# Kernel optimization log

Measured on AMD Instinct MI355X. Metric: run time of the kernel, lower is better.

Reference implementation:

```python
import jax, jax.numpy as jnp
import numpy as np

B, S, D, H = 4, 2048, 1024, 16
DEPTH = D // H
NEG = 1e10


def setup_inputs() -> dict:
    key = jax.random.key(0)
    ks = jax.random.split(key, 11)
    sc = 0.02
    return {
        "q": jax.random.normal(ks[0], (B, S, D), jnp.float32),
        "v": jax.random.normal(ks[1], (B, S, D), jnp.float32),
        "k": jax.random.normal(ks[2], (B, S, D), jnp.float32),
        "Wq": jax.random.normal(ks[3], (D, D), jnp.float32) * sc,
        "bq": jnp.zeros((D,), jnp.float32),
        "Wk": jax.random.normal(ks[4], (D, D), jnp.float32) * sc,
        "bk": jnp.zeros((D,), jnp.float32),
        "Wv": jax.random.normal(ks[5], (D, D), jnp.float32) * sc,
        "bv": jnp.zeros((D,), jnp.float32),
        "Wo": jax.random.normal(ks[6], (D, D), jnp.float32) * sc,
        "bo": jnp.zeros((D,), jnp.float32),
        "mask": 1,
    }


def _split_heads(x):
    # [B, S, D] -> [B, H, S, depth]
    b, s, _ = x.shape
    return x.reshape(b, s, H, DEPTH).transpose(0, 2, 1, 3)


def reference(q, v, k, Wq, bq, Wk, bk, Wv, bv, Wo, bo, mask):
    qh = _split_heads(q @ Wq + bq)
    kh = _split_heads(k @ Wk + bk)
    vh = _split_heads(v @ Wv + bv)

    scale = 1.0 / jnp.sqrt(jnp.asarray(DEPTH, jnp.float32))
    # [B, H, Sq, Sk]
    logits = jnp.einsum("bhqd,bhkd->bhqk", qh, kh) * scale

    if mask:
        nd, ns = logits.shape[-2], logits.shape[-1]
        i = jnp.arange(nd)[:, None]
        j = jnp.arange(ns)[None, :]
        b = (i >= j - ns + nd).astype(logits.dtype)  # lower triangle from lower-right
        logits = logits * b - NEG * (1.0 - b)

    attn = jax.nn.softmax(logits, axis=-1)
    out = jnp.einsum("bhqk,bhkd->bhqd", attn, vh)  # [B, H, Sq, depth]
    out = out.transpose(0, 2, 1, 3).reshape(q.shape[0], -1, D)  # concat heads
    return out @ Wo + bo
```

## Files before the change

### kernel.cpp

```cpp
#include <hip/hip_runtime.h>
#include <hip/hip_bf16.h>
#include <cstdint>
#include <cstddef>

#define S_LEN 2048
#define D_MODEL 1024
#define N_HEADS 16
#define DEPTH 64
#define BATCH 4

#define GLOBAL_AS __attribute__((address_space(1)))
#define LDS_AS __attribute__((address_space(3)))

typedef __attribute__((ext_vector_type(4))) float f32x4;
typedef __attribute__((ext_vector_type(8))) short bf16x8;
typedef __attribute__((ext_vector_type(4))) unsigned short us4;
typedef __attribute__((ext_vector_type(8))) unsigned short us8;

__device__ __forceinline__ unsigned short f2bf(float f) {
  unsigned int u = __builtin_bit_cast(unsigned int, f);
  u += 0x7FFFu + ((u >> 16) & 1u);
  return (unsigned short)(u >> 16);
}

__device__ __forceinline__ unsigned short f2bf_hw(float f) {
  return __builtin_bit_cast(unsigned short, __float2bfloat16(f));
}

__global__ __launch_bounds__(256) void transpose_cast(const float* __restrict__ W,
                                                      unsigned short* __restrict__ Wt,
                                                      int N, float scale) {
  __shared__ float tile[32][33];
  int bx = blockIdx.x * 32;
  int by = blockIdx.y * 32;
  int tx = threadIdx.x, ty = threadIdx.y;
#pragma unroll
  for (int i = 0; i < 4; ++i)
    tile[ty + i * 8][tx] = W[(size_t)(by + ty + i * 8) * N + bx + tx];
  __syncthreads();
#pragma unroll
  for (int i = 0; i < 4; ++i)
    Wt[(size_t)(bx + ty + i * 8) * N + by + tx] = f2bf(tile[tx][ty + i * 8] * scale);
}

__global__ __launch_bounds__(256) void transpose_v(const unsigned short* __restrict__ Vp,
                                                   unsigned short* __restrict__ Vt) {
  __shared__ unsigned short tile[64][72];
  int tid = threadIdx.x;
  int sb = blockIdx.x;
  int bh = blockIdx.y;
  int b = bh >> 4, h = bh & 15;
  int s0 = sb * 64;
#pragma unroll
  for (int rep = 0; rep < 2; ++rep) {
    int idx = rep * 256 + tid;
    int r = idx >> 3, c8 = idx & 7;
    us8 v = *(const us8*)(Vp + (size_t)(b * S_LEN + s0 + r) * D_MODEL + h * DEPTH + c8 * 8);
#pragma unroll
    for (int e = 0; e < 8; ++e) tile[c8 * 8 + e][r] = v[e];
  }
  __syncthreads();
#pragma unroll
  for (int rep = 0; rep < 2; ++rep) {
    int idx = rep * 256 + tid;
    int d = idx >> 3, c8 = idx & 7;
    us8 v = *(const us8*)&tile[d][c8 * 8];
    *(us8*)(Vt + ((size_t)(bh * DEPTH + d)) * S_LEN + s0 + c8 * 8) = v;
  }
}

struct GemmSlice {
  const void* A;
  const unsigned short* Bt;
  const float* bias;
  void* C;
  float bscale;
};
struct GemmArgs {
  GemmSlice s[3];
};

template <bool A_IS_F32, bool OUT_F32>
__global__ __launch_bounds__(256) void gemm_bt(GemmArgs args, int M, int N, int K) {
  constexpr int ASTR = A_IS_F32 ? 72 : 64;
  __shared__ unsigned short a_lds[2][128 * ASTR];
  __shared__ unsigned short b_lds[2][128 * 64];

  const GemmSlice& g = args.s[blockIdx.y];
  const float* Af = (const float*)g.A;
  const unsigned short* Ah = (const unsigned short*)g.A;
  const unsigned short* Bt = g.Bt;

  int tid = threadIdx.x;
  int wave = tid >> 6, lane = tid & 63;
  int l15 = lane & 15, lg = lane >> 4;
  int wm = wave >> 1, wn = wave & 1;

  int d = blockIdx.x;
  int wk = (d & 7) * 64 + (d >> 3);
  int mi = (wk >> 6) * 8 + ((wk & 63) >> 3);
  int nj = wk & 7;
  int row0 = mi * 128, col0 = nj * 128;

  f32x4 acc[4][4] = {};
  f32x4 av[8];

  int ar = tid >> 4, ac4 = tid & 15;

  auto loadA = [&](int k0) {
#pragma unroll
    for (int rep = 0; rep < 8; ++rep)
      av[rep] = *(const f32x4*)(Af + (size_t)(row0 + rep * 16 + ar) * K + k0 + ac4 * 4);
  };
  auto writeA = [&](int buf) {
#pragma unroll
    for (int rep = 0; rep < 8; ++rep) {
      us4 h = {f2bf_hw(av[rep][0]), f2bf_hw(av[rep][1]),
               f2bf_hw(av[rep][2]), f2bf_hw(av[rep][3])};
      *(us4*)&a_lds[buf][(rep * 16 + ar) * 72 + ac4 * 4] = h;
    }
  };
  auto issueA = [&](int buf, int k0) {
#pragma unroll
    for (int rep = 0; rep < 4; ++rep) {
      int chunk = (wave * 4 + rep) * 64 + lane;
      int row = chunk >> 3;
      int c8 = (chunk & 7) ^ (row & 7);
      __builtin_amdgcn_global_load_lds(
          (const GLOBAL_AS void*)(Ah + (size_t)(row0 + row) * K + k0 + c8 * 8),
          (LDS_AS void*)(&a_lds[buf][chunk * 8]), 16, 0, 0);
    }
  };
  auto issueB = [&](int buf, int k0) {
#pragma unroll
    for (int rep = 0; rep < 4; ++rep) {
      int chunk = (wave * 4 + rep) * 64 + lane;
      int row = chunk >> 3;
      int c8 = (chunk & 7) ^ (row & 7);
      __builtin_amdgcn_global_load_lds(
          (const GLOBAL_AS void*)(Bt + (size_t)(col0 + row) * K + k0 + c8 * 8),
          (LDS_AS void*)(&b_lds[buf][chunk * 8]), 16, 0, 0);
    }
  };
  auto compute = [&](int buf) {
#pragma unroll
    for (int kk = 0; kk < 2; ++kk) {
      bf16x8 af[4], bfr[4];
#pragma unroll
      for (int ii = 0; ii < 4; ++ii) {
        int row = wm * 64 + ii * 16 + l15;
        if constexpr (A_IS_F32)
          af[ii] = *(const bf16x8*)&a_lds[buf][row * 72 + kk * 32 + lg * 8];
        else
          af[ii] = *(const bf16x8*)&a_lds[buf][row * 64 + ((kk * 4 + lg) ^ (l15 & 7)) * 8];
      }
#pragma unroll
      for (int jj = 0; jj < 4; ++jj) {
        int row = wn * 64 + jj * 16 + l15;
        bfr[jj] = *(const bf16x8*)&b_lds[buf][row * 64 + ((kk * 4 + lg) ^ (l15 & 7)) * 8];
      }
#pragma unroll
      for (int ii = 0; ii < 4; ++ii)
#pragma unroll
        for (int jj = 0; jj < 4; ++jj)
          acc[ii][jj] = __builtin_amdgcn_mfma_f32_16x16x32_bf16(af[ii], bfr[jj], acc[ii][jj], 0, 0, 0);
    }
  };

  int nk = K >> 6;
  issueB(0, 0);
  if constexpr (A_IS_F32) {
    loadA(0);
    writeA(0);
  } else {
    issueA(0, 0);
  }

  for (int ki = 0; ki < nk; ++ki) {
    int cur = ki & 1;
    __syncthreads();
    bool more = (ki + 1) < nk;
    if (more) {
      issueB(cur ^ 1, (ki + 1) * 64);
      if constexpr (A_IS_F32)
        loadA((ki + 1) * 64);
      else
        issueA(cur ^ 1, (ki + 1) * 64);
    }
    compute(cur);
    if (more) {
      if constexpr (A_IS_F32) writeA(cur ^ 1);
    }
  }

#pragma unroll
  for (int ii = 0; ii < 4; ++ii) {
#pragma unroll
    for (int jj = 0; jj < 4; ++jj) {
      int col = col0 + wn * 64 + jj * 16 + l15;
      float bv = g.bias[col] * g.bscale;
#pragma unroll
      for (int r = 0; r < 4; ++r) {
        int row = row0 + wm * 64 + ii * 16 + lg * 4 + r;
        float v = acc[ii][jj][r] + bv;
        if constexpr (OUT_F32)
          ((float*)g.C)[(size_t)row * N + col] = v;
        else
          ((unsigned short*)g.C)[(size_t)row * N + col] = f2bf(v);
      }
    }
  }
}

__global__ __launch_bounds__(512) void attn_kernel(const unsigned short* __restrict__ Qp,
                                                   const unsigned short* __restrict__ Kp,
                                                   const unsigned short* __restrict__ Vt,
                                                   unsigned short* __restrict__ Op) {
  __shared__ unsigned short k_lds[2][64][76];
  __shared__ unsigned short vt_lds[2][64][76];
  __shared__ unsigned short p_lds[8][16][76];

  int tid = threadIdx.x;
  int w = tid >> 6, lane = tid & 63;
  int l15 = lane & 15, lg = lane >> 4;

  int bid = blockIdx.x;
  int swz = (bid & 7) * 64 + (bid >> 3);
  int pairIdx = swz & 7;
  int bh = swz >> 3;
  int b = bh >> 4, h = bh & 15;

  const unsigned short* Kbase = Kp + (size_t)b * S_LEN * D_MODEL + h * DEPTH;
  const unsigned short* Vbase = Vt + (size_t)bh * DEPTH * S_LEN;

  bool stageV = (tid >= 256);
  int st = tid & 255;
  int r = st >> 2, cb = (st & 3) * 16;
  const unsigned short* srow = stageV ? (Vbase + (size_t)r * S_LEN + cb)
                                      : (Kbase + (size_t)r * D_MODEL + cb);
  const size_t sstep = stageV ? 64 : (size_t)64 * D_MODEL;

  bf16x8 ones;
#pragma unroll
  for (int e = 0; e < 8; ++e) ones[e] = (short)0x3F80;

  for (int half = 0; half < 2; ++half) {
    int t = (half == 0) ? pairIdx : (15 - pairIdx);
    int q0 = t * 128;
    int nkv = 2 * t + 2;
    int q0w = q0 + w * 16;

    const unsigned short* qp =
        Qp + ((size_t)(b * S_LEN + q0 + w * 16 + l15)) * D_MODEL + h * DEPTH;
    bf16x8 qf0 = *(const bf16x8*)(qp + lg * 8);
    bf16x8 qf1 = *(const bf16x8*)(qp + 32 + lg * 8);

    f32x4 acc_l = (f32x4){0.f, 0.f, 0.f, 0.f};
    f32x4 acc_o[4];
#pragma unroll
    for (int dd = 0; dd < 4; ++dd) acc_o[dd] = (f32x4){0.f, 0.f, 0.f, 0.f};

    const unsigned short* sptr = srow;
    us8 s0 = *(const us8*)sptr;
    us8 s1 = *(const us8*)(sptr + 8);
    sptr += sstep;
    __syncthreads();
    if (stageV) {
      *(us8*)&vt_lds[0][r][cb] = s0;
      *(us8*)&vt_lds[0][r][cb + 8] = s1;
    } else {
      *(us8*)&k_lds[0][r][cb] = s0;
      *(us8*)&k_lds[0][r][cb + 8] = s1;
    }

    for (int kb = 0; kb < nkv; ++kb) {
      int cur = kb & 1;
      int k0 = kb * 64;
      __syncthreads();
      bool more = (kb + 1) < nkv;
      if (more) {
        s0 = *(const us8*)sptr;
        s1 = *(const us8*)(sptr + 8);
        sptr += sstep;
      }

      bool full_masked = (k0 > q0w + 15);
      if (!full_masked) {
        f32x4 s[4];
#pragma unroll
        for (int nf = 0; nf < 4; ++nf) s[nf] = (f32x4){0.f, 0.f, 0.f, 0.f};
        __builtin_amdgcn_s_setprio(1);
#pragma unroll
        for (int nf = 0; nf < 4; ++nf) {
          bf16x8 kf0 = *(const bf16x8*)&k_lds[cur][nf * 16 + l15][lg * 8];
          bf16x8 kf1 = *(const bf16x8*)&k_lds[cur][nf * 16 + l15][32 + lg * 8];
          s[nf] = __builtin_amdgcn_mfma_f32_16x16x32_bf16(qf0, kf0, s[nf], 0, 0, 0);
          s[nf] = __builtin_amdgcn_mfma_f32_16x16x32_bf16(qf1, kf1, s[nf], 0, 0, 0);
        }
        __builtin_amdgcn_s_setprio(0);

        bool diag = (k0 + 63 > q0w);
        if (diag) {
#pragma unroll
          for (int nf = 0; nf < 4; ++nf)
#pragma unroll
            for (int rr = 0; rr < 4; ++rr) {
              int qrow = q0w + lg * 4 + rr;
              int kcol = k0 + nf * 16 + l15;
              float x = (kcol > qrow) ? -1e10f : s[nf][rr];
              float p = __builtin_amdgcn_exp2f(x);
              p_lds[w][lg * 4 + rr][nf * 16 + l15] =
                  (unsigned short)(__builtin_bit_cast(unsigned int, p) >> 16);
            }
        } else {
#pragma unroll
          for (int nf = 0; nf < 4; ++nf)
#pragma unroll
            for (int rr = 0; rr < 4; ++rr) {
              float p = __builtin_amdgcn_exp2f(s[nf][rr]);
              p_lds[w][lg * 4 + rr][nf * 16 + l15] =
                  (unsigned short)(__builtin_bit_cast(unsigned int, p) >> 16);
            }
        }

        __builtin_amdgcn_s_setprio(1);
#pragma unroll
        for (int kk = 0; kk < 2; ++kk) {
          bf16x8 pf = *(const bf16x8*)&p_lds[w][l15][kk * 32 + lg * 8];
          acc_l = __builtin_amdgcn_mfma_f32_16x16x32_bf16(pf, ones, acc_l, 0, 0, 0);
#pragma unroll
          for (int dd = 0; dd < 4; ++dd) {
            bf16x8 vf = *(const bf16x8*)&vt_lds[cur][dd * 16 + l15][kk * 32 + lg * 8];
            acc_o[dd] = __builtin_amdgcn_mfma_f32_16x16x32_bf16(pf, vf, acc_o[dd], 0, 0, 0);
          }
        }
        __builtin_amdgcn_s_setprio(0);
      }

      if (more) {
        int nb = cur ^ 1;
        if (stageV) {
          *(us8*)&vt_lds[nb][r][cb] = s0;
          *(us8*)&vt_lds[nb][r][cb + 8] = s1;
        } else {
          *(us8*)&k_lds[nb][r][cb] = s0;
          *(us8*)&k_lds[nb][r][cb + 8] = s1;
        }
      }
    }

#pragma unroll
    for (int rr = 0; rr < 4; ++rr) {
      float inv = 1.0f / acc_l[rr];
      int qrow = q0 + w * 16 + lg * 4 + rr;
      unsigned short* op = Op + ((size_t)(b * S_LEN + qrow)) * D_MODEL + h * DEPTH;
#pragma unroll
      for (int dd = 0; dd < 4; ++dd)
        op[dd * 16 + l15] = f2bf(acc_o[dd][rr] * inv);
    }
  }
}

extern "C" void kernel_launch(void* const* d_in, const int* in_sizes, int n_in,
                              void* d_out, int out_size, void* d_ws, size_t ws_size,
                              hipStream_t stream) {
  const float* q  = (const float*)d_in[0];
  const float* v  = (const float*)d_in[1];
  const float* k  = (const float*)d_in[2];
  const float* Wq = (const float*)d_in[3];
  const float* bq = (const float*)d_in[4];
  const float* Wk = (const float*)d_in[5];
  const float* bk = (const float*)d_in[6];
  const float* Wv = (const float*)d_in[7];
  const float* bv = (const float*)d_in[8];
  const float* Wo = (const float*)d_in[9];
  const float* bo = (const float*)d_in[10];

  char* ws = (char*)d_ws;
  const size_t WSZ = (size_t)D_MODEL * D_MODEL * 2;
  const size_t XSZ = (size_t)BATCH * S_LEN * D_MODEL * 2;
  unsigned short* Wqt = (unsigned short*)(ws);
  unsigned short* Wkt = (unsigned short*)(ws + WSZ);
  unsigned short* Wvt = (unsigned short*)(ws + 2 * WSZ);
  unsigned short* Wot = (unsigned short*)(ws + 3 * WSZ);
  unsigned short* Qp  = (unsigned short*)(ws + 4 * WSZ);
  unsigned short* Kp  = (unsigned short*)(ws + 4 * WSZ + XSZ);
  unsigned short* Vp  = (unsigned short*)(ws + 4 * WSZ + 2 * XSZ);
  unsigned short* Vtp = (unsigned short*)(ws + 4 * WSZ + 3 * XSZ);
  unsigned short* AO  = Vp;

  const float SCL = 0.125f * 1.4426950408889634f;
  const int M = BATCH * S_LEN;

  dim3 tb(32, 8);
  dim3 tg(D_MODEL / 32, D_MODEL / 32);
  hipLaunchKernelGGL(transpose_cast, tg, tb, 0, stream, Wq, Wqt, D_MODEL, SCL);
  hipLaunchKernelGGL(transpose_cast, tg, tb, 0, stream, Wk, Wkt, D_MODEL, 1.0f);
  hipLaunchKernelGGL(transpose_cast, tg, tb, 0, stream, Wv, Wvt, D_MODEL, 1.0f);
  hipLaunchKernelGGL(transpose_cast, tg, tb, 0, stream, Wo, Wot, D_MODEL, 1.0f);

  GemmArgs qkv{};
  qkv.s[0] = GemmSlice{(const void*)q, Wqt, bq, (void*)Qp, SCL};
  qkv.s[1] = GemmSlice{(const void*)k, Wkt, bk, (void*)Kp, 1.0f};
  qkv.s[2] = GemmSlice{(const void*)v, Wvt, bv, (void*)Vp, 1.0f};
  hipLaunchKernelGGL((gemm_bt<true, false>), dim3(512, 3), dim3(256), 0, stream,
                     qkv, M, D_MODEL, D_MODEL);

  hipLaunchKernelGGL(transpose_v, dim3(S_LEN / 64, BATCH * N_HEADS), dim3(256), 0, stream,
                     Vp, Vtp);

  hipLaunchKernelGGL(attn_kernel, dim3(512), dim3(512), 0, stream, Qp, Kp, Vtp, AO);

  GemmArgs ao{};
  ao.s[0] = GemmSlice{(const void*)AO, Wot, bo, d_out, 1.0f};
  hipLaunchKernelGGL((gemm_bt<false, true>), dim3(512, 1), dim3(256), 0, stream,
                     ao, M, D_MODEL, D_MODEL);
}
```

Measured before the change: 185.6 us.

## Drop LDS double buffering in GEMM and attention, raise occupancy hints

Both the GEMM and attention kernels move from double-buffered LDS tiles to single buffers, with an extra barrier per iteration around the staging writes. Launch-bound occupancy hints (4 blocks for the GEMM, 8 for attention) are added to fit more resident waves, and the GEMM grid drops its swizzled tile order for a plain (M/128, slices×8) layout. The aim is to trade software pipelining for higher occupancy and smaller LDS use, at the risk of exposing load latency and losing L2 locality from the removed swizzle.

New measurement: 460.5 us. 2.48x slower.

```diff
diff --git a/kernel.cpp b/kernel.cpp
--- a/kernel.cpp
+++ b/kernel.cpp
@@ -81,12 +81,14 @@
 };
 
 template <bool A_IS_F32, bool OUT_F32>
-__global__ __launch_bounds__(256) void gemm_bt(GemmArgs args, int M, int N, int K) {
+__global__ __launch_bounds__(256, 4) void gemm_bt(GemmArgs args, int M, int N, int K) {
   constexpr int ASTR = A_IS_F32 ? 72 : 64;
-  __shared__ unsigned short a_lds[2][128 * ASTR];
-  __shared__ unsigned short b_lds[2][128 * 64];
-
-  const GemmSlice& g = args.s[blockIdx.y];
+  __shared__ unsigned short a_lds[128 * ASTR];
+  __shared__ unsigned short b_lds[128 * 64];
+
+  int slice = blockIdx.y >> 3;
+  int nj = blockIdx.y & 7;
+  const GemmSlice& g = args.s[slice];
   const float* Af = (const float*)g.A;
   const unsigned short* Ah = (const unsigned short*)g.A;
   const unsigned short* Bt = g.Bt;
@@ -96,11 +98,8 @@
   int l15 = lane & 15, lg = lane >> 4;
   int wm = wave >> 1, wn = wave & 1;
 
-  int d = blockIdx.x;
-  int wk = (d & 7) * 64 + (d >> 3);
-  int mi = (wk >> 6) * 8 + ((wk & 63) >> 3);
-  int nj = wk & 7;
-  int row0 = mi * 128, col0 = nj * 128;
+  int row0 = blockIdx.x * 128;
+  int col0 = nj * 128;
 
   f32x4 acc[4][4] = {};
   f32x4 av[8];
@@ -112,15 +111,15 @@
     for (int rep = 0; rep < 8; ++rep)
       av[rep] = *(const f32x4*)(Af + (size_t)(row0 + rep * 16 + ar) * K + k0 + ac4 * 4);
   };
-  auto writeA = [&](int buf) {
+  auto writeA = [&]() {
 #pragma unroll
     for (int rep = 0; rep < 8; ++rep) {
       us4 h = {f2bf_hw(av[rep][0]), f2bf_hw(av[rep][1]),
                f2bf_hw(av[rep][2]), f2bf_hw(av[rep][3])};
-      *(us4*)&a_lds[buf][(rep * 16 + ar) * 72 + ac4 * 4] = h;
-    }
-  };
-  auto issueA = [&](int buf, int k0) {
+      *(us4*)&a_lds[(rep * 16 + ar) * 72 + ac4 * 4] = h;
+    }
+  };
+  auto issueA = [&](int k0) {
 #pragma unroll
     for (int rep = 0; rep < 4; ++rep) {
       int chunk = (wave * 4 + rep) * 64 + lane;
@@ -128,10 +127,10 @@
       int c8 = (chunk & 7) ^ (row & 7);
       __builtin_amdgcn_global_load_lds(
           (const GLOBAL_AS void*)(Ah + (size_t)(row0 + row) * K + k0 + c8 * 8),
-          (LDS_AS void*)(&a_lds[buf][chunk * 8]), 16, 0, 0);
-    }
-  };
-  auto issueB = [&](int buf, int k0) {
+          (LDS_AS void*)(&a_lds[chunk * 8]), 16, 0, 0);
+    }
+  };
+  auto issueB = [&](int k0) {
 #pragma unroll
     for (int rep = 0; rep < 4; ++rep) {
       int chunk = (wave * 4 + rep) * 64 + lane;
@@ -139,10 +138,10 @@
       int c8 = (chunk & 7) ^ (row & 7);
       __builtin_amdgcn_global_load_lds(
           (const GLOBAL_AS void*)(Bt + (size_t)(col0 + row) * K + k0 + c8 * 8),
-          (LDS_AS void*)(&b_lds[buf][chunk * 8]), 16, 0, 0);
-    }
-  };
-  auto compute = [&](int buf) {
+          (LDS_AS void*)(&b_lds[chunk * 8]), 16, 0, 0);
+    }
+  };
+  auto compute = [&]() {
 #pragma unroll
     for (int kk = 0; kk < 2; ++kk) {
       bf16x8 af[4], bfr[4];
@@ -150,14 +149,14 @@
       for (int ii = 0; ii < 4; ++ii) {
         int row = wm * 64 + ii * 16 + l15;
         if constexpr (A_IS_F32)
-          af[ii] = *(const bf16x8*)&a_lds[buf][row * 72 + kk * 32 + lg * 8];
+          af[ii] = *(const bf16x8*)&a_lds[row * 72 + kk * 32 + lg * 8];
         else
-          af[ii] = *(const bf16x8*)&a_lds[buf][row * 64 + ((kk * 4 + lg) ^ (l15 & 7)) * 8];
+          af[ii] = *(const bf16x8*)&a_lds[row * 64 + (((kk * 4 + lg) ^ (l15 & 7)) * 8)];
       }
 #pragma unroll
       for (int jj = 0; jj < 4; ++jj) {
         int row = wn * 64 + jj * 16 + l15;
-        bfr[jj] = *(const bf16x8*)&b_lds[buf][row * 64 + ((kk * 4 + lg) ^ (l15 & 7)) * 8];
+        bfr[jj] = *(const bf16x8*)&b_lds[row * 64 + (((kk * 4 + lg) ^ (l15 & 7)) * 8)];
       }
 #pragma unroll
       for (int ii = 0; ii < 4; ++ii)
@@ -168,29 +167,20 @@
   };
 
   int nk = K >> 6;
-  issueB(0, 0);
-  if constexpr (A_IS_F32) {
-    loadA(0);
-    writeA(0);
-  } else {
-    issueA(0, 0);
-  }
+  if constexpr (A_IS_F32) loadA(0);
 
   for (int ki = 0; ki < nk; ++ki) {
-    int cur = ki & 1;
     __syncthreads();
-    bool more = (ki + 1) < nk;
-    if (more) {
-      issueB(cur ^ 1, (ki + 1) * 64);
-      if constexpr (A_IS_F32)
-        loadA((ki + 1) * 64);
-      else
-        issueA(cur ^ 1, (ki + 1) * 64);
-    }
-    compute(cur);
-    if (more) {
-      if constexpr (A_IS_F32) writeA(cur ^ 1);
-    }
+    issueB(ki * 64);
+    if constexpr (A_IS_F32)
+      writeA();
+    else
+      issueA(ki * 64);
+    __syncthreads();
+    if constexpr (A_IS_F32) {
+      if (ki + 1 < nk) loadA((ki + 1) * 64);
+    }
+    compute();
   }
 
 #pragma unroll
@@ -212,12 +202,12 @@
   }
 }
 
-__global__ __launch_bounds__(512) void attn_kernel(const unsigned short* __restrict__ Qp,
-                                                   const unsigned short* __restrict__ Kp,
-                                                   const unsigned short* __restrict__ Vt,
-                                                   unsigned short* __restrict__ Op) {
-  __shared__ unsigned short k_lds[2][64][76];
-  __shared__ unsigned short vt_lds[2][64][76];
+__global__ __launch_bounds__(512, 8) void attn_kernel(const unsigned short* __restrict__ Qp,
+                                                      const unsigned short* __restrict__ Kp,
+                                                      const unsigned short* __restrict__ Vt,
+                                                      unsigned short* __restrict__ Op) {
+  __shared__ unsigned short k_lds[64][76];
+  __shared__ unsigned short vt_lds[64][76];
   __shared__ unsigned short p_lds[8][16][76];
 
   int tid = threadIdx.x;
@@ -264,18 +254,17 @@
     us8 s0 = *(const us8*)sptr;
     us8 s1 = *(const us8*)(sptr + 8);
     sptr += sstep;
-    __syncthreads();
-    if (stageV) {
-      *(us8*)&vt_lds[0][r][cb] = s0;
-      *(us8*)&vt_lds[0][r][cb + 8] = s1;
-    } else {
-      *(us8*)&k_lds[0][r][cb] = s0;
-      *(us8*)&k_lds[0][r][cb + 8] = s1;
-    }
 
     for (int kb = 0; kb < nkv; ++kb) {
-      int cur = kb & 1;
       int k0 = kb * 64;
+      __syncthreads();
+      if (stageV) {
+        *(us8*)&vt_lds[r][cb] = s0;
+        *(us8*)&vt_lds[r][cb + 8] = s1;
+      } else {
+        *(us8*)&k_lds[r][cb] = s0;
+        *(us8*)&k_lds[r][cb + 8] = s1;
+      }
       __syncthreads();
       bool more = (kb + 1) < nkv;
       if (more) {
@@ -292,8 +281,8 @@
         __builtin_amdgcn_s_setprio(1);
 #pragma unroll
         for (int nf = 0; nf < 4; ++nf) {
-          bf16x8 kf0 = *(const bf16x8*)&k_lds[cur][nf * 16 + l15][lg * 8];
-          bf16x8 kf1 = *(const bf16x8*)&k_lds[cur][nf * 16 + l15][32 + lg * 8];
+          bf16x8 kf0 = *(const bf16x8*)&k_lds[nf * 16 + l15][lg * 8];
+          bf16x8 kf1 = *(const bf16x8*)&k_lds[nf * 16 + l15][32 + lg * 8];
           s[nf] = __builtin_amdgcn_mfma_f32_16x16x32_bf16(qf0, kf0, s[nf], 0, 0, 0);
           s[nf] = __builtin_amdgcn_mfma_f32_16x16x32_bf16(qf1, kf1, s[nf], 0, 0, 0);
         }
@@ -330,22 +319,11 @@
           acc_l = __builtin_amdgcn_mfma_f32_16x16x32_bf16(pf, ones, acc_l, 0, 0, 0);
 #pragma unroll
           for (int dd = 0; dd < 4; ++dd) {
-            bf16x8 vf = *(const bf16x8*)&vt_lds[cur][dd * 16 + l15][kk * 32 + lg * 8];
+            bf16x8 vf = *(const bf16x8*)&vt_lds[dd * 16 + l15][kk * 32 + lg * 8];
             acc_o[dd] = __builtin_amdgcn_mfma_f32_16x16x32_bf16(pf, vf, acc_o[dd], 0, 0, 0);
           }
         }
         __builtin_amdgcn_s_setprio(0);
-      }
-
-      if (more) {
-        int nb = cur ^ 1;
-        if (stageV) {
-          *(us8*)&vt_lds[nb][r][cb] = s0;
-          *(us8*)&vt_lds[nb][r][cb + 8] = s1;
-        } else {
-          *(us8*)&k_lds[nb][r][cb] = s0;
-          *(us8*)&k_lds[nb][r][cb + 8] = s1;
-        }
       }
     }
 
@@ -403,7 +381,7 @@
   qkv.s[0] = GemmSlice{(const void*)q, Wqt, bq, (void*)Qp, SCL};
   qkv.s[1] = GemmSlice{(const void*)k, Wkt, bk, (void*)Kp, 1.0f};
   qkv.s[2] = GemmSlice{(const void*)v, Wvt, bv, (void*)Vp, 1.0f};
-  hipLaunchKernelGGL((gemm_bt<true, false>), dim3(512, 3), dim3(256), 0, stream,
+  hipLaunchKernelGGL((gemm_bt<true, false>), dim3(M / 128, 24), dim3(256), 0, stream,
                      qkv, M, D_MODEL, D_MODEL);
 
   hipLaunchKernelGGL(transpose_v, dim3(S_LEN / 64, BATCH * N_HEADS), dim3(256), 0, stream,
@@ -413,6 +391,6 @@
 
   GemmArgs ao{};
   ao.s[0] = GemmSlice{(const void*)AO, Wot, bo, d_out, 1.0f};
-  hipLaunchKernelGGL((gemm_bt<false, true>), dim3(512, 1), dim3(256), 0, stream,
+  hipLaunchKernelGGL((gemm_bt<false, true>), dim3(M / 128, 8), dim3(256), 0, stream,
                      ao, M, D_MODEL, D_MODEL);
 }
```
